# Optimization experiments

Hardware: AMD Instinct MI355X
Metric: run time of the kernel (lower is better)

## Reference

```python
import jax, jax.numpy as jnp
import numpy as np

N_NODES = 100000
N_FEAT = 256
HIDDEN = 16
N_CLASSES = 16
N_EDGES = 3200000


def setup_inputs() -> dict:
    key = jax.random.key(0)
    k = jax.random.split(key, 7)
    x = jax.random.normal(k[0], (N_NODES, N_FEAT), dtype=jnp.float32)
    edge_index = jax.random.randint(k[1], (2, N_EDGES), 0, N_NODES, dtype=jnp.int32)
    # GCNConv: linear (no bias) + bias added after aggregation
    s1 = 1.0 / np.sqrt(N_FEAT)
    W1 = jax.random.uniform(k[2], (N_FEAT, HIDDEN), jnp.float32, -s1, s1)
    b1 = jnp.zeros((HIDDEN,), jnp.float32)
    # SAGEConv: lin_l (on aggregated neighbors, with bias) + lin_r (root)
    s2 = 1.0 / np.sqrt(HIDDEN)
    Wl = jax.random.uniform(k[3], (HIDDEN, N_CLASSES), jnp.float32, -s2, s2)
    Wr = jax.random.uniform(k[4], (HIDDEN, N_CLASSES), jnp.float32, -s2, s2)
    b2 = jax.random.uniform(k[5], (N_CLASSES,), jnp.float32, -s2, s2)
    return {"x": x, "edge_index": edge_index, "W1": W1, "b1": b1,
            "Wl": Wl, "Wr": Wr, "b2": b2}


def reference(x, edge_index, W1, b1, Wl, Wr, b2):
    N = x.shape[0]
    src, dst = edge_index[0], edge_index[1]

    # ---- GCNConv(num_features -> hidden): transform, add self-loops,
    # symmetric normalization, sum-aggregate, add bias ----
    h = x @ W1  # [N, H]
    loop = jnp.arange(N, dtype=src.dtype)
    src2 = jnp.concatenate([src, loop])
    dst2 = jnp.concatenate([dst, loop])
    ones = jnp.ones(src2.shape[0], dtype=h.dtype)
    deg = jax.ops.segment_sum(ones, dst2, num_segments=N)  # in-degree incl. self-loop
    dinv = jnp.where(deg > 0, jax.lax.rsqrt(deg), 0.0)
    norm = dinv[src2] * dinv[dst2]  # [E+N]
    msgs = h[src2] * norm[:, None]
    h1 = jax.ops.segment_sum(msgs, dst2, num_segments=N) + b1  # [N, H]

    # ---- SAGEConv(hidden -> num_classes, aggr='mean') ----
    cnt = jax.ops.segment_sum(jnp.ones(src.shape[0], dtype=h1.dtype), dst, num_segments=N)
    agg = jax.ops.segment_sum(h1[src], dst, num_segments=N)
    agg = agg / jnp.maximum(cnt, 1.0)[:, None]  # mean over neighbors
    out = agg @ Wl + h1 @ Wr + b2  # [N, C]

    return jax.nn.log_softmax(out, axis=1)
```

## Files before the change

### kernel.cpp

```cpp
#include <hip/hip_runtime.h>
#include <cstddef>

#define NF 256
#define NH 16
#define NC 16

#define BN    128
#define BSH   7
#define BMSK  127
#define CAP   4608
#define AVLEN 16
#define ACH   (256*AVLEN)
#define NBMAX 800

typedef __attribute__((ext_vector_type(8))) short bf16x8;
typedef __attribute__((ext_vector_type(4))) float f32x4;

__device__ inline short f2bf(float f) {
    union { float f; unsigned int u; } v; v.f = f;
    const unsigned int r = v.u + 0x7FFFu + ((v.u >> 16) & 1u);
    return (short)(r >> 16);
}
__device__ inline float bf2f(unsigned short u) {
    union { unsigned int i; float f; } v; v.i = ((unsigned int)u) << 16;
    return v.f;
}

__global__ __launch_bounds__(256) void fusedAG_kernel(
    const int* __restrict__ src, const int* __restrict__ dst,
    unsigned int* __restrict__ bfill, unsigned int* __restrict__ bpairs,
    const float* __restrict__ x, const float* __restrict__ W1,
    float* __restrict__ hs_u, int E, int NBK, int NCH, int GEMMB, int N)
{
    __shared__ unsigned int hist[NBMAX];
    __shared__ unsigned int sbase[NBMAX];
    __shared__ unsigned int gpos[NBMAX];
    __shared__ unsigned int tmp[1024];
    __shared__ unsigned int reorder[ACH];
    __shared__ unsigned short wbid[ACH];

    const int tid = threadIdx.x;

    const int nInter = 2 * (NCH < GEMMB ? NCH : GEMMB);
    int msId = -1, gbId = -1;
    const int bi = (int)blockIdx.x;
    if (bi < nInter) {
        if (bi & 1) gbId = bi >> 1; else msId = bi >> 1;
    } else {
        const int r = bi - nInter;
        if (NCH > GEMMB) msId = (nInter >> 1) + r; else gbId = (nInter >> 1) + r;
    }

    if (msId >= 0) {
        for (int i = tid; i < NBMAX; i += 256) hist[i] = 0u;
        __syncthreads();

        const int base = msId * ACH;
        unsigned int pv[AVLEN];
        unsigned int ps[AVLEN];
        #pragma unroll
        for (int l = 0; l < AVLEN; ++l) {
            const int e = base + l * 256 + tid;
            if (e < E) {
                const unsigned int s = (unsigned int)src[e];
                const unsigned int d = (unsigned int)dst[e];
                const unsigned int b = d >> BSH;
                pv[l] = (s << BSH) | (d & BMSK);
                const unsigned int slot = atomicAdd(&hist[b], 1u);
                ps[l] = (slot << 10) | b;
            } else {
                ps[l] = 0xFFFFFFFFu;
            }
        }
        __syncthreads();

        for (int i = tid; i < 1024; i += 256) tmp[i] = (i < NBK) ? hist[i] : 0u;
        __syncthreads();
        for (int off = 1; off < 1024; off <<= 1) {
            unsigned int v0 = 0, v1 = 0, v2 = 0, v3 = 0;
            const int i0 = tid, i1 = tid + 256, i2 = tid + 512, i3 = tid + 768;
            if (i0 >= off) v0 = tmp[i0 - off];
            if (i1 >= off) v1 = tmp[i1 - off];
            if (i2 >= off) v2 = tmp[i2 - off];
            if (i3 >= off) v3 = tmp[i3 - off];
            __syncthreads();
            tmp[i0] += v0; tmp[i1] += v1; tmp[i2] += v2; tmp[i3] += v3;
            __syncthreads();
        }
        for (int i = tid; i < NBK; i += 256) {
            const unsigned int h = hist[i];
            sbase[i] = tmp[i] - h;
            if (h) gpos[i] = atomicAdd(&bfill[i], h);
        }
        const int cc = (base + ACH <= E) ? ACH : (E - base);
        __syncthreads();

        #pragma unroll
        for (int l = 0; l < AVLEN; ++l) {
            if (ps[l] != 0xFFFFFFFFu) {
                const unsigned int b = ps[l] & 1023u;
                const unsigned int i = sbase[b] + (ps[l] >> 10);
                reorder[i] = pv[l];
                wbid[i] = (unsigned short)b;
            }
        }
        __syncthreads();

        for (int i = tid; i < cc; i += 256) {
            const unsigned int b = wbid[i];
            const unsigned int g = gpos[b] + ((unsigned int)i - sbase[b]);
            if (g < CAP) bpairs[(size_t)b * CAP + g] = reorder[i];
        }
    } else {
        const int lane = tid & 63;
        const int wave = tid >> 6;
        const int quad = lane >> 4;
        const int mn   = lane & 15;

        bf16x8 bfrag[8];
        #pragma unroll
        for (int kc = 0; kc < 8; ++kc) {
            #pragma unroll
            for (int j = 0; j < 8; ++j) {
                const int k = kc * 32 + quad * 8 + j;
                bfrag[kc][j] = f2bf(W1[k * NH + mn]);
            }
        }

        #pragma unroll
        for (int t = 0; t < 2; ++t) {
            const int tile = gbId * 8 + wave * 2 + t;
            const int n0 = tile * 16;
            if (n0 >= N) break;

            f32x4 acc = {0.f, 0.f, 0.f, 0.f};
            const float* xrow = x + (size_t)(n0 + mn) * NF + quad * 8;
            #pragma unroll
            for (int kc = 0; kc < 8; ++kc) {
                const float4 lo = *(const float4*)(xrow + kc * 32);
                const float4 hi = *(const float4*)(xrow + kc * 32 + 4);
                bf16x8 af;
                af[0] = f2bf(lo.x); af[1] = f2bf(lo.y); af[2] = f2bf(lo.z); af[3] = f2bf(lo.w);
                af[4] = f2bf(hi.x); af[5] = f2bf(hi.y); af[6] = f2bf(hi.z); af[7] = f2bf(hi.w);
                acc = __builtin_amdgcn_mfma_f32_16x16x32_bf16(af, bfrag[kc], acc, 0, 0, 0);
            }

            #pragma unroll
            for (int r = 0; r < 4; ++r) {
                const int row = quad * 4 + r;
                hs_u[(size_t)(n0 + row) * NH + mn] = acc[r];
            }
        }
    }
}

__global__ __launch_bounds__(256) void bucketB_kernel(
    const unsigned int* __restrict__ bfill, unsigned int* __restrict__ bpairs,
    const float* __restrict__ hs_u,
    int* __restrict__ rowptr, int* __restrict__ cnt, float* __restrict__ dinv,
    unsigned short* __restrict__ hs_bf, int N)
{
    __shared__ unsigned int pairs[CAP];
    __shared__ unsigned int ssorted[CAP];
    __shared__ unsigned int hist[BN];
    __shared__ unsigned int scan[BN];
    __shared__ unsigned int cursor[BN];
    __shared__ float sdinv[BN];

    const int tid = threadIdx.x;
    const int b = blockIdx.x;
    const size_t bbase = (size_t)b * CAP;
    const int nodeBase = b * BN;
    unsigned int m = bfill[b]; if (m > CAP) m = CAP;

    if (tid < BN) hist[tid] = 0u;
    __syncthreads();

    for (unsigned int i = tid; i < m; i += 256) {
        const unsigned int p = bpairs[bbase + i];
        pairs[i] = p;
        atomicAdd(&hist[p & BMSK], 1u);
    }
    __syncthreads();

    if (tid < BN) scan[tid] = hist[tid];
    __syncthreads();
    for (int off = 1; off < BN; off <<= 1) {
        unsigned int v = 0;
        if (tid < BN && tid >= off) v = scan[tid - off];
        __syncthreads();
        if (tid < BN) scan[tid] += v;
        __syncthreads();
    }
    if (tid < BN) cursor[tid] = scan[tid] - hist[tid];
    __syncthreads();

    for (unsigned int i = tid; i < m; i += 256) {
        const unsigned int p = pairs[i];
        const unsigned int pos = atomicAdd(&cursor[p & BMSK], 1u);
        ssorted[pos] = p >> BSH;
    }
    __syncthreads();

    for (unsigned int i = tid; i < m; i += 256)
        bpairs[bbase + i] = ssorted[i];

    if (tid < BN) {
        const int n = nodeBase + tid;
        const unsigned int h = hist[tid];
        const float dv = rsqrtf((float)h + 1.0f);
        sdinv[tid] = dv;
        if (n < N) {
            cnt[n] = (int)h;
            dinv[n] = dv;
            rowptr[n] = (int)(b * CAP + (scan[tid] - h));
        }
    }
    __syncthreads();

    for (int t = tid; t < BN * NH; t += 256) {
        const int n = nodeBase + (t >> 4);
        if (n < N) {
            const size_t idx = (size_t)n * NH + (t & 15);
            hs_bf[idx] = (unsigned short)f2bf(hs_u[idx] * sdinv[t >> 4]);
        }
    }
}

__global__ __launch_bounds__(256) void gcn_gather_kernel(
    const unsigned short* __restrict__ hs_bf, const unsigned int* __restrict__ csrc,
    const int* __restrict__ rowptr, const int* __restrict__ cnt,
    const float* __restrict__ dinv, const float* __restrict__ b1,
    unsigned short* __restrict__ h1_bf, int N)
{
    const int tid = threadIdx.x;
    const int n = blockIdx.x * 16 + (tid >> 4);
    if (n >= N) return;
    const int j = tid & 15;
    const int start = rowptr[n];
    const int end = start + cnt[n];

    float acc = bf2f(hs_bf[(size_t)n * NH + j]);
    for (int k = start; k < end; k += 16) {
        const int idx = k + j;
        const int myi = (int)csrc[idx < end ? idx : (end - 1)];
        const int rem = end - k;
        if (rem >= 16) {
            float s = 0.f;
            #pragma unroll
            for (int u = 0; u < 16; ++u) {
                const int sidx = __shfl(myi, u, 16);
                s += bf2f(hs_bf[(size_t)sidx * NH + j]);
            }
            acc += s;
        } else {
            float s = 0.f;
            #pragma unroll
            for (int u = 0; u < 16; ++u) {
                const int sidx = __shfl(myi, u, 16);
                const float v = bf2f(hs_bf[(size_t)sidx * NH + j]);
                s += (u < rem) ? v : 0.f;
            }
            acc += s;
        }
    }

    h1_bf[(size_t)n * NH + j] = (unsigned short)f2bf(b1[j] + dinv[n] * acc);
}

__global__ __launch_bounds__(256) void sage_out_kernel(
    const unsigned short* __restrict__ h1_bf, const unsigned int* __restrict__ csrc,
    const int* __restrict__ rowptr, const int* __restrict__ cnt,
    const float* __restrict__ Wl, const float* __restrict__ Wr,
    const float* __restrict__ b2, float* __restrict__ out, int N)
{
    __shared__ float wls[NH * NC];
    __shared__ float wrs[NH * NC];
    __shared__ float b2s[NC];
    const int tid = threadIdx.x;
    if (tid < NH * NC) { wls[tid] = Wl[tid]; wrs[tid] = Wr[tid]; }
    if (tid < NC) b2s[tid] = b2[tid];
    __syncthreads();

    const int n = blockIdx.x * 16 + (tid >> 4);
    if (n >= N) return;
    const int j = tid & 15;
    const int start = rowptr[n];
    const int deg = cnt[n];
    const int end = start + deg;

    float acc = 0.f;
    for (int k = start; k < end; k += 16) {
        const int idx = k + j;
        const int myi = (int)csrc[idx < end ? idx : (end - 1)];
        const int rem = end - k;
        if (rem >= 16) {
            float s = 0.f;
            #pragma unroll
            for (int u = 0; u < 16; ++u) {
                const int sidx = __shfl(myi, u, 16);
                s += bf2f(h1_bf[(size_t)sidx * NH + j]);
            }
            acc += s;
        } else {
            float s = 0.f;
            #pragma unroll
            for (int u = 0; u < 16; ++u) {
                const int sidx = __shfl(myi, u, 16);
                const float v = bf2f(h1_bf[(size_t)sidx * NH + j]);
                s += (u < rem) ? v : 0.f;
            }
            acc += s;
        }
    }

    const float aggj = acc / fmaxf((float)deg, 1.0f);
    const float h1j  = bf2f(h1_bf[(size_t)n * NH + j]);

    float o = b2s[j];
    #pragma unroll
    for (int kk = 0; kk < NH; ++kk) {
        const float a  = __shfl(aggj, kk, 16);
        const float hh = __shfl(h1j,  kk, 16);
        o += a * wls[kk * NC + j] + hh * wrs[kk * NC + j];
    }

    float m = o;
    #pragma unroll
    for (int off = 1; off < 16; off <<= 1) m = fmaxf(m, __shfl_xor(m, off, 16));
    const float ex = expf(o - m);
    float ssum = ex;
    #pragma unroll
    for (int off = 1; off < 16; off <<= 1) ssum += __shfl_xor(ssum, off, 16);

    out[(size_t)n * NC + j] = (o - m) - logf(ssum);
}

extern "C" void kernel_launch(void* const* d_in, const int* in_sizes, int n_in,
                              void* d_out, int out_size, void* d_ws, size_t ws_size,
                              hipStream_t stream)
{
    const float* x  = (const float*)d_in[0];
    const int*   ei = (const int*)d_in[1];
    const float* W1 = (const float*)d_in[2];
    const float* b1 = (const float*)d_in[3];
    const float* Wl = (const float*)d_in[4];
    const float* Wr = (const float*)d_in[5];
    const float* b2 = (const float*)d_in[6];
    float* out = (float*)d_out;

    const int N = in_sizes[0] / NF;
    const int E = in_sizes[1] / 2;
    const int* src = ei;
    const int* dst = ei + E;

    const int NBK = (N + BN - 1) / BN;
    const int NCH = (E + ACH - 1) / ACH;
    const int tiles = (N + 15) / 16;
    const int GEMMB = (tiles + 7) / 8;

    unsigned short* hs_bf = (unsigned short*)d_ws;
    unsigned short* h1_bf = hs_bf + (size_t)N * NH;
    float* hs_u   = (float*)(h1_bf + (size_t)N * NH);
    float* dinv   = hs_u + (size_t)N * NH;
    int*   cnt    = (int*)(dinv + N);
    int*   rowptr = cnt + N;
    unsigned int* bfill  = (unsigned int*)(rowptr + N);
    unsigned int* bpairs = bfill + 1024;

    hipMemsetAsync(bfill, 0, (size_t)NBK * sizeof(unsigned int), stream);

    fusedAG_kernel<<<NCH + GEMMB, 256, 0, stream>>>(
        src, dst, bfill, bpairs, x, W1, hs_u, E, NBK, NCH, GEMMB, N);
    bucketB_kernel<<<NBK, 256, 0, stream>>>(
        bfill, bpairs, hs_u, rowptr, cnt, dinv, hs_bf, N);

    const int nodeBlk = (N + 15) / 16;
    gcn_gather_kernel<<<nodeBlk, 256, 0, stream>>>(hs_bf, bpairs, rowptr, cnt, dinv, b1, h1_bf, N);
    sage_out_kernel<<<nodeBlk, 256, 0, stream>>>(h1_bf, bpairs, rowptr, cnt, Wl, Wr, b2, out, N);
}
```

Before: 278.5 us.

## Fuse GCN gather into bucket sort kernel; compute degrees via global atomics

Result: slower. 369.7 us (+32.7%).

```diff
diff --git a/kernel.cpp b/kernel.cpp
--- a/kernel.cpp
+++ b/kernel.cpp
@@ -29,6 +29,7 @@
 __global__ __launch_bounds__(256) void fusedAG_kernel(
     const int* __restrict__ src, const int* __restrict__ dst,
     unsigned int* __restrict__ bfill, unsigned int* __restrict__ bpairs,
+    int* __restrict__ cnt,
     const float* __restrict__ x, const float* __restrict__ W1,
     float* __restrict__ hs_u, int E, int NBK, int NCH, int GEMMB, int N)
 {
@@ -68,6 +69,7 @@
                 pv[l] = (s << BSH) | (d & BMSK);
                 const unsigned int slot = atomicAdd(&hist[b], 1u);
                 ps[l] = (slot << 10) | b;
+                atomicAdd(&cnt[d], 1);
             } else {
                 ps[l] = 0xFFFFFFFFu;
             }
@@ -154,18 +156,35 @@
     }
 }
 
-__global__ __launch_bounds__(256) void bucketB_kernel(
+__global__ __launch_bounds__(256) void scale_kernel(
+    const float* __restrict__ hs_u, const int* __restrict__ cnt,
+    float* __restrict__ dinv, unsigned short* __restrict__ hs_bf, int N)
+{
+    const int t = blockIdx.x * 256 + threadIdx.x;
+    const int e4 = t * 4;
+    if (e4 >= N * NH) return;
+    const int n = e4 >> 4;
+    const float dv = rsqrtf((float)cnt[n] + 1.0f);
+    const float4 v = *(const float4*)(hs_u + e4);
+    ushort4 r;
+    r.x = (unsigned short)f2bf(v.x * dv);
+    r.y = (unsigned short)f2bf(v.y * dv);
+    r.z = (unsigned short)f2bf(v.z * dv);
+    r.w = (unsigned short)f2bf(v.w * dv);
+    *(ushort4*)(hs_bf + e4) = r;
+    if ((e4 & 15) == 0) dinv[n] = dv;
+}
+
+__global__ __launch_bounds__(256) void bucketB_gcn_kernel(
     const unsigned int* __restrict__ bfill, unsigned int* __restrict__ bpairs,
-    const float* __restrict__ hs_u,
-    int* __restrict__ rowptr, int* __restrict__ cnt, float* __restrict__ dinv,
-    unsigned short* __restrict__ hs_bf, int N)
+    const unsigned short* __restrict__ hs_bf, const float* __restrict__ b1,
+    int* __restrict__ rowptr, unsigned short* __restrict__ h1_bf, int N)
 {
     __shared__ unsigned int pairs[CAP];
     __shared__ unsigned int ssorted[CAP];
     __shared__ unsigned int hist[BN];
     __shared__ unsigned int scan[BN];
     __shared__ unsigned int cursor[BN];
-    __shared__ float sdinv[BN];
 
     const int tid = threadIdx.x;
     const int b = blockIdx.x;
@@ -204,68 +223,51 @@
 
     for (unsigned int i = tid; i < m; i += 256)
         bpairs[bbase + i] = ssorted[i];
-
     if (tid < BN) {
         const int n = nodeBase + tid;
-        const unsigned int h = hist[tid];
-        const float dv = rsqrtf((float)h + 1.0f);
-        sdinv[tid] = dv;
-        if (n < N) {
-            cnt[n] = (int)h;
-            dinv[n] = dv;
-            rowptr[n] = (int)(b * CAP + (scan[tid] - h));
-        }
-    }
-    __syncthreads();
-
-    for (int t = tid; t < BN * NH; t += 256) {
-        const int n = nodeBase + (t >> 4);
-        if (n < N) {
-            const size_t idx = (size_t)n * NH + (t & 15);
-            hs_bf[idx] = (unsigned short)f2bf(hs_u[idx] * sdinv[t >> 4]);
-        }
-    }
-}
-
-__global__ __launch_bounds__(256) void gcn_gather_kernel(
-    const unsigned short* __restrict__ hs_bf, const unsigned int* __restrict__ csrc,
-    const int* __restrict__ rowptr, const int* __restrict__ cnt,
-    const float* __restrict__ dinv, const float* __restrict__ b1,
-    unsigned short* __restrict__ h1_bf, int N)
-{
-    const int tid = threadIdx.x;
-    const int n = blockIdx.x * 16 + (tid >> 4);
-    if (n >= N) return;
+        if (n < N) rowptr[n] = (int)(b * CAP + (scan[tid] - hist[tid]));
+    }
+    __syncthreads();
+
+    const int g = tid >> 4;
     const int j = tid & 15;
-    const int start = rowptr[n];
-    const int end = start + cnt[n];
-
-    float acc = bf2f(hs_bf[(size_t)n * NH + j]);
-    for (int k = start; k < end; k += 16) {
-        const int idx = k + j;
-        const int myi = (int)csrc[idx < end ? idx : (end - 1)];
-        const int rem = end - k;
-        if (rem >= 16) {
-            float s = 0.f;
-            #pragma unroll
-            for (int u = 0; u < 16; ++u) {
-                const int sidx = __shfl(myi, u, 16);
-                s += bf2f(hs_bf[(size_t)sidx * NH + j]);
-            }
-            acc += s;
-        } else {
-            float s = 0.f;
-            #pragma unroll
-            for (int u = 0; u < 16; ++u) {
-                const int sidx = __shfl(myi, u, 16);
-                const float v = bf2f(hs_bf[(size_t)sidx * NH + j]);
-                s += (u < rem) ? v : 0.f;
-            }
-            acc += s;
-        }
-    }
-
-    h1_bf[(size_t)n * NH + j] = (unsigned short)f2bf(b1[j] + dinv[n] * acc);
+    const float b1j = b1[j];
+
+    for (int t = 0; t < 8; ++t) {
+        const int ln = g * 8 + t;
+        const int n = nodeBase + ln;
+        if (n >= N) continue;
+        const int deg  = (int)hist[ln];
+        const int base = (int)(scan[ln] - hist[ln]);
+        const float dv = rsqrtf((float)deg + 1.0f);
+
+        float acc = bf2f(hs_bf[(size_t)n * NH + j]);
+        for (int k = 0; k < deg; k += 16) {
+            const int kj = k + j;
+            const int myi = (int)ssorted[base + (kj < deg ? kj : deg - 1)];
+            const int rem = deg - k;
+            if (rem >= 16) {
+                float s = 0.f;
+                #pragma unroll
+                for (int u = 0; u < 16; ++u) {
+                    const int sidx = __shfl(myi, u, 16);
+                    s += bf2f(hs_bf[(size_t)sidx * NH + j]);
+                }
+                acc += s;
+            } else {
+                float s = 0.f;
+                #pragma unroll
+                for (int u = 0; u < 16; ++u) {
+                    const int sidx = __shfl(myi, u, 16);
+                    const float v = bf2f(hs_bf[(size_t)sidx * NH + j]);
+                    s += (u < rem) ? v : 0.f;
+                }
+                acc += s;
+            }
+        }
+
+        h1_bf[(size_t)n * NH + j] = (unsigned short)f2bf(b1j + dv * acc);
+    }
 }
 
 __global__ __launch_bounds__(256) void sage_out_kernel(
@@ -363,19 +365,22 @@
     unsigned short* h1_bf = hs_bf + (size_t)N * NH;
     float* hs_u   = (float*)(h1_bf + (size_t)N * NH);
     float* dinv   = hs_u + (size_t)N * NH;
-    int*   cnt    = (int*)(dinv + N);
-    int*   rowptr = cnt + N;
+    int*   rowptr = (int*)(dinv + N);
     unsigned int* bfill  = (unsigned int*)(rowptr + N);
-    unsigned int* bpairs = bfill + 1024;
-
-    hipMemsetAsync(bfill, 0, (size_t)NBK * sizeof(unsigned int), stream);
+    int*   cnt    = (int*)(bfill + 1024);
+    unsigned int* bpairs = (unsigned int*)(cnt + N);
+
+    hipMemsetAsync(bfill, 0, (size_t)(1024 + N) * sizeof(unsigned int), stream);
 
     fusedAG_kernel<<<NCH + GEMMB, 256, 0, stream>>>(
-        src, dst, bfill, bpairs, x, W1, hs_u, E, NBK, NCH, GEMMB, N);
-    bucketB_kernel<<<NBK, 256, 0, stream>>>(
-        bfill, bpairs, hs_u, rowptr, cnt, dinv, hs_bf, N);
+        src, dst, bfill, bpairs, cnt, x, W1, hs_u, E, NBK, NCH, GEMMB, N);
+
+    const int scaleBlk = (N * NH / 4 + 255) / 256;
+    scale_kernel<<<scaleBlk, 256, 0, stream>>>(hs_u, cnt, dinv, hs_bf, N);
+
+    bucketB_gcn_kernel<<<NBK, 256, 0, stream>>>(
+        bfill, bpairs, hs_bf, b1, rowptr, h1_bf, N);
 
     const int nodeBlk = (N + 15) / 16;
-    gcn_gather_kernel<<<nodeBlk, 256, 0, stream>>>(hs_bf, bpairs, rowptr, cnt, dinv, b1, h1_bf, N);
     sage_out_kernel<<<nodeBlk, 256, 0, stream>>>(h1_bf, bpairs, rowptr, cnt, Wl, Wr, b2, out, N);
 }
```
